# Optimization experiments

Hardware: AMD Instinct MI355X
Metric: run time of the kernel (lower is better)

The kernel has to match this reference:

```python
import jax, jax.numpy as jnp
import numpy as np

N = 129      # num_of_nodes hardcoded in EvolveGCNH(129, in_channels)
IN = 129     # in_channels; must satisfy ceil(IN/129 * N) == IN for GRU shapes
OUT = 64     # out_channels of final linear
E = 4096     # number of edges (avg degree ~32)


def setup_inputs() -> dict:
    key = jax.random.key(0)
    ks = jax.random.split(key, 12)
    s = 1.0 / np.sqrt(IN)
    x = jax.random.normal(ks[0], (N, IN), jnp.float32)
    edge_index = jax.random.randint(ks[1], (2, E), 0, N)
    edge_weight = jax.random.uniform(ks[2], (E,), jnp.float32, minval=0.1, maxval=1.0)
    # TopKPooling projection vector p
    pool_p = jax.random.normal(ks[3], (IN,), jnp.float32) * s
    # initial GCN weight (GRU hidden state), glorot-ish
    W0 = jax.random.normal(ks[4], (IN, IN), jnp.float32) * s
    # GRU parameters (torch layout: rows ordered [reset; update; new])
    w_ih = jax.random.normal(ks[5], (3 * IN, IN), jnp.float32) * s
    w_hh = jax.random.normal(ks[6], (3 * IN, IN), jnp.float32) * s
    b_ih = jax.random.normal(ks[7], (3 * IN,), jnp.float32) * s
    b_hh = jax.random.normal(ks[8], (3 * IN,), jnp.float32) * s
    conv_bias = jax.random.normal(ks[9], (IN,), jnp.float32) * s
    lin_w = jax.random.normal(ks[10], (OUT, IN), jnp.float32) * s
    lin_b = jax.random.normal(ks[11], (OUT,), jnp.float32) * s
    return {"x": x, "edge_index": edge_index, "edge_weight": edge_weight,
            "pool_p": pool_p, "W0": W0, "w_ih": w_ih, "w_hh": w_hh,
            "b_ih": b_ih, "b_hh": b_hh, "conv_bias": conv_bias,
            "lin_w": lin_w, "lin_b": lin_b}


def reference(x, edge_index, edge_weight, pool_p, W0, w_ih, w_hh, b_ih, b_hh,
              conv_bias, lin_w, lin_b):
    n = x.shape[0]
    # F.dropout in eval mode (training=False) -> identity.

    # --- TopKPooling: score = tanh(x @ p / ||p||); select top-k (k == IN == N) ---
    score = jnp.tanh((x @ pool_p) / jnp.linalg.norm(pool_p))
    perm = jnp.argsort(-score)                     # descending, k = IN = n
    x_tilde = x[perm] * score[perm][:, None]       # [k, IN]

    # --- GRU step: input batch = k pooled nodes, hidden = evolving weight W0 [IN, IN] ---
    gi = x_tilde @ w_ih.T + b_ih                   # [k, 3*IN]
    gh = W0 @ w_hh.T + b_hh                        # [IN, 3*IN]
    ir, iz, i_n = jnp.split(gi, 3, axis=1)
    hr, hz, h_n = jnp.split(gh, 3, axis=1)
    r = jax.nn.sigmoid(ir + hr)
    z = jax.nn.sigmoid(iz + hz)
    cand = jnp.tanh(i_n + r * h_n)
    W = (1.0 - z) * cand + z * W0                  # evolved GCN weight [IN, IN]

    # --- GCNConv_Fixed_W: gcn_norm with self-loops, then D^-1/2 A D^-1/2 (x @ W) ---
    row, col = edge_index[0], edge_index[1]        # source, target
    loop = jnp.arange(n)
    row_f = jnp.concatenate([row, loop])
    col_f = jnp.concatenate([col, loop])
    ew_f = jnp.concatenate([edge_weight, jnp.ones((n,), x.dtype)])
    deg = jax.ops.segment_sum(ew_f, col_f, num_segments=n)
    dis = jnp.where(deg > 0, jax.lax.rsqrt(jnp.maximum(deg, 1e-12)), 0.0)
    norm = dis[row_f] * ew_f * dis[col_f]          # [E+n]
    xw = x @ W                                     # [N, IN]
    out = jax.ops.segment_sum(norm[:, None] * xw[row_f], col_f, num_segments=n)
    out = out + conv_bias

    # --- ELU + Linear ---
    h = jax.nn.elu(out)
    return h @ lin_w.T + lin_b
```

## Files before the change

### kernel.cpp

```cpp
#include <hip/hip_runtime.h>
#include <math.h>

#define NN 129
#define INC 129
#define OUTC 64
#define NE 4096
#define WCAP 32

__device__ __forceinline__ float sigmf(float x) { return 1.0f / (1.0f + expf(-x)); }

__global__ __launch_bounds__(1024) void k_prep(
    const float* __restrict__ x, const int* __restrict__ ei,
    const float* __restrict__ ew, const float* __restrict__ p,
    float* __restrict__ score, int* __restrict__ perm, float* __restrict__ agg)
{
    int b = blockIdx.x, t = threadIdx.x;
    int wv = t >> 6, lane = t & 63;
    const int* row = ei;
    const int* col = ei + NE;

    if (b == 0) {
        __shared__ float s_sc[NN];

        float pv0 = p[lane];
        float pv1 = p[lane + 64];
        float pv2 = p[128];
        float pn = pv0 * pv0 + pv1 * pv1;
        if (lane == 0) pn += pv2 * pv2;

        float acc[9];
        #pragma unroll
        for (int k = 0; k < 9; ++k) {
            int n = wv + k * 16;
            float a = 0.f;
            if (n < NN) {
                const float* xr = x + (size_t)n * INC;
                a = xr[lane] * pv0 + xr[lane + 64] * pv1;
                if (lane == 0) a += xr[128] * pv2;
            }
            acc[k] = a;
        }
        #pragma unroll
        for (int o = 32; o; o >>= 1) {
            #pragma unroll
            for (int k = 0; k < 9; ++k) acc[k] += __shfl_xor(acc[k], o, 64);
            pn += __shfl_xor(pn, o, 64);
        }
        float rinv = 1.0f / sqrtf(pn);
        if (lane == 0) {
            #pragma unroll
            for (int k = 0; k < 9; ++k) {
                int n = wv + k * 16;
                if (n < NN) s_sc[n] = acc[k];
            }
        }
        __syncthreads();
        if (t < NN) {
            float sc = tanhf(s_sc[t] * rinv);
            s_sc[t] = sc;
            score[t] = sc;
        }
        __syncthreads();
        if (t < NN) {
            float my = s_sc[t];
            int rank = 0;
            #pragma unroll 16
            for (int j = 0; j < NN; ++j) {
                float o = s_sc[j];
                rank += (o > my || (o == my && j < t)) ? 1 : 0;
            }
            perm[rank] = t;
        }
    } else {
        int c = b - 1;
        __shared__ float s_deg[NN];
        __shared__ float s_dis[NN];
        __shared__ int   s_r[16 * WCAP];
        __shared__ float s_w[16 * WCAP];
        __shared__ int   s_cnt[16];
        __shared__ int   s_off[17];
        __shared__ int   s_dr[16 * WCAP];
        __shared__ float s_nrm[16 * WCAP];

        if (t < NN) s_deg[t] = 0.f;
        __syncthreads();
        for (int e = t; e < NE; e += 1024) atomicAdd(&s_deg[col[e]], ew[e]);
        __syncthreads();
        if (t < NN) s_dis[t] = rsqrtf(fmaxf(s_deg[t] + 1.0f, 1e-12f));
        __syncthreads();

        int basee = wv * 256;
        int cnt = 0;
        #pragma unroll
        for (int it = 0; it < 4; ++it) {
            int e = basee + it * 64 + lane;
            int rr = row[e];
            float wval = ew[e];
            bool m = (col[e] == c);
            unsigned long long mask = __ballot(m);
            if (m) {
                int pos = cnt + __popcll(mask & ((1ull << lane) - 1));
                if (pos < WCAP) { s_r[wv * WCAP + pos] = rr; s_w[wv * WCAP + pos] = wval; }
            }
            cnt += __popcll(mask);
        }
        if (lane == 0) s_cnt[wv] = min(cnt, WCAP);
        __syncthreads();
        if (t == 0) {
            int acc = 0;
            for (int w = 0; w < 16; ++w) { s_off[w] = acc; acc += s_cnt[w]; }
            s_off[16] = acc;
        }
        __syncthreads();
        float dc = s_dis[c];
        if (lane < s_cnt[wv]) {
            int r = s_r[wv * WCAP + lane];
            s_dr[s_off[wv] + lane]  = r;
            s_nrm[s_off[wv] + lane] = s_dis[r] * s_w[wv * WCAP + lane] * dc;
        }
        __syncthreads();
        int tot = s_off[16];
        if (t < NN) {
            float a = dc * dc * x[(size_t)c * INC + t];
            #pragma unroll 8
            for (int k = 0; k < tot; ++k)
                a += s_nrm[k] * x[(size_t)s_dr[k] * INC + t];
            agg[(size_t)c * INC + t] = a;
        }
    }
}

__global__ __launch_bounds__(256) void k_gru(
    const float* __restrict__ x, const float* __restrict__ score,
    const int* __restrict__ perm, const float* __restrict__ W0,
    const float* __restrict__ w_ih, const float* __restrict__ w_hh,
    const float* __restrict__ b_ih, const float* __restrict__ b_hh,
    float* __restrict__ W)
{
    int lane = threadIdx.x & 63;
    int wid = blockIdx.x * 4 + (threadIdx.x >> 6);
    if (wid >= NN * INC) return;
    int j = wid / NN;
    int i = wid - j * NN;
    int pi = perm[i];
    float sc = score[pi];
    const float* xr = x  + (size_t)pi * INC;
    const float* h0 = W0 + (size_t)i * INC;
    const float* wr = w_ih + (size_t)j * INC;
    const float* wz = wr + (size_t)INC * INC;
    const float* wn = wz + (size_t)INC * INC;
    const float* vr = w_hh + (size_t)j * INC;
    const float* vz = vr + (size_t)INC * INC;
    const float* vn = vz + (size_t)INC * INC;

    float sr = 0.f, szv = 0.f, an = 0.f, hn = 0.f;
    for (int c = lane; c < INC; c += 64) {
        float xv = xr[c] * sc;
        float hv = h0[c];
        sr  += xv * wr[c] + hv * vr[c];
        szv += xv * wz[c] + hv * vz[c];
        an  += xv * wn[c];
        hn  += hv * vn[c];
    }
    for (int o = 32; o; o >>= 1) {
        sr  += __shfl_xor(sr,  o, 64);
        szv += __shfl_xor(szv, o, 64);
        an  += __shfl_xor(an,  o, 64);
        hn  += __shfl_xor(hn,  o, 64);
    }
    if (lane == 0) {
        float r    = sigmf(sr  + b_ih[j]           + b_hh[j]);
        float z    = sigmf(szv + b_ih[INC + j]     + b_hh[INC + j]);
        float cand = tanhf(an + b_ih[2 * INC + j] + r * (hn + b_hh[2 * INC + j]));
        W[(size_t)i * INC + j] = (1.0f - z) * cand + z * h0[j];
    }
}

__global__ __launch_bounds__(1024) void k_fin(
    const float* __restrict__ agg, const float* __restrict__ W,
    const float* __restrict__ cb, const float* __restrict__ lw,
    const float* __restrict__ lb, float* __restrict__ out)
{
    __shared__ float s_a[NN];
    __shared__ float s_g[NN];
    __shared__ float s_h[NN];
    int c = blockIdx.x, t = threadIdx.x;
    int wv = t >> 6, lane = t & 63;

    if (t < NN) { s_a[t] = agg[(size_t)c * INC + t]; s_g[t] = cb[t]; }
    __syncthreads();

    float p0 = 0.f, p1 = 0.f, p2 = 0.f;
    for (int cc = wv; cc < NN; cc += 16) {
        float av = s_a[cc];
        const float* wr = W + (size_t)cc * INC;
        p0 += av * wr[lane];
        p1 += av * wr[lane + 64];
        if (lane == 0) p2 += av * wr[128];
    }
    atomicAdd(&s_g[lane], p0);
    atomicAdd(&s_g[lane + 64], p1);
    if (lane == 0) atomicAdd(&s_g[128], p2);
    __syncthreads();
    if (t < NN) { float g = s_g[t]; s_h[t] = (g > 0.f) ? g : expm1f(g); }
    __syncthreads();

    for (int f = wv; f < OUTC; f += 16) {
        const float* wrow = lw + (size_t)f * INC;
        float a = 0.f;
        for (int cc = lane; cc < INC; cc += 64) a += s_h[cc] * wrow[cc];
        for (int o = 32; o; o >>= 1) a += __shfl_xor(a, o, 64);
        if (lane == 0) out[(size_t)c * OUTC + f] = a + lb[f];
    }
}

extern "C" void kernel_launch(void* const* d_in, const int* in_sizes, int n_in,
                              void* d_out, int out_size, void* d_ws, size_t ws_size,
                              hipStream_t stream)
{
    const float* x   = (const float*)d_in[0];
    const int*   ei  = (const int*)d_in[1];
    const float* ew  = (const float*)d_in[2];
    const float* pp  = (const float*)d_in[3];
    const float* W0  = (const float*)d_in[4];
    const float* wih = (const float*)d_in[5];
    const float* whh = (const float*)d_in[6];
    const float* bih = (const float*)d_in[7];
    const float* bhh = (const float*)d_in[8];
    const float* cb  = (const float*)d_in[9];
    const float* lw  = (const float*)d_in[10];
    const float* lb  = (const float*)d_in[11];
    float* out = (float*)d_out;

    char* ws = (char*)d_ws;
    float* score = (float*)(ws + 0);
    int*   perm  = (int*)  (ws + 640);
    float* W     = (float*)(ws + 2048);
    float* agg   = (float*)(ws + 2048 + 69632);

    k_prep<<<NN + 1, 1024, 0, stream>>>(x, ei, ew, pp, score, perm, agg);

    int gru_blocks = (NN * INC + 3) / 4;
    k_gru<<<gru_blocks, 256, 0, stream>>>(x, score, perm, W0, wih, whh, bih, bhh, W);

    k_fin<<<NN, 1024, 0, stream>>>(agg, W, cb, lw, lb, out);
}
```

Measured before the change: 32.57 us.

## Move aggregation into GRU kernel and use half-wave dot products for GRU

The score/top-k step now runs as its own single-block kernel. The graph aggregation blocks are merged into the GRU launch, with 256-thread blocks instead of 1024. The GRU dot products now use 32 lanes per (i,j) output instead of a full 64-lane wave, which halves idle lanes for the 129-length reductions. Aggregation now has 4 waves each scanning 1024 edges, with the per-wave edge cap raised to 64, and the score kernel becomes a separate serial launch.

```diff
diff --git a/kernel.cpp b/kernel.cpp
--- a/kernel.cpp
+++ b/kernel.cpp
@@ -5,94 +5,106 @@
 #define INC 129
 #define OUTC 64
 #define NE 4096
-#define WCAP 32
+#define WCAP 64
+#define GRU_HW_PER_BLK 8
+#define GRU_BLKS ((NN * INC + GRU_HW_PER_BLK - 1) / GRU_HW_PER_BLK)
 
 __device__ __forceinline__ float sigmf(float x) { return 1.0f / (1.0f + expf(-x)); }
 
-__global__ __launch_bounds__(1024) void k_prep(
+__global__ __launch_bounds__(1024) void k_score(
+    const float* __restrict__ x, const float* __restrict__ p,
+    float* __restrict__ score, int* __restrict__ perm)
+{
+    int t = threadIdx.x;
+    int wv = t >> 6, lane = t & 63;
+    __shared__ float s_sc[NN];
+
+    float pv0 = p[lane];
+    float pv1 = p[lane + 64];
+    float pv2 = p[128];
+    float pn = pv0 * pv0 + pv1 * pv1;
+    if (lane == 0) pn += pv2 * pv2;
+
+    float acc[9];
+    #pragma unroll
+    for (int k = 0; k < 9; ++k) {
+        int n = wv + k * 16;
+        float a = 0.f;
+        if (n < NN) {
+            const float* xr = x + (size_t)n * INC;
+            a = xr[lane] * pv0 + xr[lane + 64] * pv1;
+            if (lane == 0) a += xr[128] * pv2;
+        }
+        acc[k] = a;
+    }
+    #pragma unroll
+    for (int o = 32; o; o >>= 1) {
+        #pragma unroll
+        for (int k = 0; k < 9; ++k) acc[k] += __shfl_xor(acc[k], o, 64);
+        pn += __shfl_xor(pn, o, 64);
+    }
+    float rinv = 1.0f / sqrtf(pn);
+    if (lane == 0) {
+        #pragma unroll
+        for (int k = 0; k < 9; ++k) {
+            int n = wv + k * 16;
+            if (n < NN) s_sc[n] = acc[k];
+        }
+    }
+    __syncthreads();
+    if (t < NN) {
+        float sc = tanhf(s_sc[t] * rinv);
+        s_sc[t] = sc;
+        score[t] = sc;
+    }
+    __syncthreads();
+    if (t < NN) {
+        float my = s_sc[t];
+        int rank = 0;
+        #pragma unroll 16
+        for (int j = 0; j < NN; ++j) {
+            float o = s_sc[j];
+            rank += (o > my || (o == my && j < t)) ? 1 : 0;
+        }
+        perm[rank] = t;
+    }
+}
+
+__global__ __launch_bounds__(256) void k_mid(
     const float* __restrict__ x, const int* __restrict__ ei,
-    const float* __restrict__ ew, const float* __restrict__ p,
-    float* __restrict__ score, int* __restrict__ perm, float* __restrict__ agg)
+    const float* __restrict__ ew, const float* __restrict__ score,
+    const int* __restrict__ perm, const float* __restrict__ W0,
+    const float* __restrict__ w_ih, const float* __restrict__ w_hh,
+    const float* __restrict__ b_ih, const float* __restrict__ b_hh,
+    float* __restrict__ W, float* __restrict__ agg)
 {
     int b = blockIdx.x, t = threadIdx.x;
     int wv = t >> 6, lane = t & 63;
     const int* row = ei;
     const int* col = ei + NE;
 
-    if (b == 0) {
-        __shared__ float s_sc[NN];
-
-        float pv0 = p[lane];
-        float pv1 = p[lane + 64];
-        float pv2 = p[128];
-        float pn = pv0 * pv0 + pv1 * pv1;
-        if (lane == 0) pn += pv2 * pv2;
-
-        float acc[9];
-        #pragma unroll
-        for (int k = 0; k < 9; ++k) {
-            int n = wv + k * 16;
-            float a = 0.f;
-            if (n < NN) {
-                const float* xr = x + (size_t)n * INC;
-                a = xr[lane] * pv0 + xr[lane + 64] * pv1;
-                if (lane == 0) a += xr[128] * pv2;
-            }
-            acc[k] = a;
-        }
-        #pragma unroll
-        for (int o = 32; o; o >>= 1) {
-            #pragma unroll
-            for (int k = 0; k < 9; ++k) acc[k] += __shfl_xor(acc[k], o, 64);
-            pn += __shfl_xor(pn, o, 64);
-        }
-        float rinv = 1.0f / sqrtf(pn);
-        if (lane == 0) {
-            #pragma unroll
-            for (int k = 0; k < 9; ++k) {
-                int n = wv + k * 16;
-                if (n < NN) s_sc[n] = acc[k];
-            }
-        }
-        __syncthreads();
-        if (t < NN) {
-            float sc = tanhf(s_sc[t] * rinv);
-            s_sc[t] = sc;
-            score[t] = sc;
-        }
-        __syncthreads();
-        if (t < NN) {
-            float my = s_sc[t];
-            int rank = 0;
-            #pragma unroll 16
-            for (int j = 0; j < NN; ++j) {
-                float o = s_sc[j];
-                rank += (o > my || (o == my && j < t)) ? 1 : 0;
-            }
-            perm[rank] = t;
-        }
-    } else {
-        int c = b - 1;
+    if (b < NN) {
+        int c = b;
         __shared__ float s_deg[NN];
         __shared__ float s_dis[NN];
-        __shared__ int   s_r[16 * WCAP];
-        __shared__ float s_w[16 * WCAP];
-        __shared__ int   s_cnt[16];
-        __shared__ int   s_off[17];
-        __shared__ int   s_dr[16 * WCAP];
-        __shared__ float s_nrm[16 * WCAP];
+        __shared__ int   s_r[4 * WCAP];
+        __shared__ float s_w[4 * WCAP];
+        __shared__ int   s_cnt[4];
+        __shared__ int   s_off[5];
+        __shared__ int   s_dr[4 * WCAP];
+        __shared__ float s_nrm[4 * WCAP];
 
         if (t < NN) s_deg[t] = 0.f;
         __syncthreads();
-        for (int e = t; e < NE; e += 1024) atomicAdd(&s_deg[col[e]], ew[e]);
+        for (int e = t; e < NE; e += 256) atomicAdd(&s_deg[col[e]], ew[e]);
         __syncthreads();
         if (t < NN) s_dis[t] = rsqrtf(fmaxf(s_deg[t] + 1.0f, 1e-12f));
         __syncthreads();
 
-        int basee = wv * 256;
+        int basee = wv * 1024;
         int cnt = 0;
         #pragma unroll
-        for (int it = 0; it < 4; ++it) {
+        for (int it = 0; it < 16; ++it) {
             int e = basee + it * 64 + lane;
             int rr = row[e];
             float wval = ew[e];
@@ -108,8 +120,8 @@
         __syncthreads();
         if (t == 0) {
             int acc = 0;
-            for (int w = 0; w < 16; ++w) { s_off[w] = acc; acc += s_cnt[w]; }
-            s_off[16] = acc;
+            for (int w = 0; w < 4; ++w) { s_off[w] = acc; acc += s_cnt[w]; }
+            s_off[4] = acc;
         }
         __syncthreads();
         float dc = s_dis[c];
@@ -119,7 +131,7 @@
             s_nrm[s_off[wv] + lane] = s_dis[r] * s_w[wv * WCAP + lane] * dc;
         }
         __syncthreads();
-        int tot = s_off[16];
+        int tot = s_off[4];
         if (t < NN) {
             float a = dc * dc * x[(size_t)c * INC + t];
             #pragma unroll 8
@@ -127,52 +139,45 @@
                 a += s_nrm[k] * x[(size_t)s_dr[k] * INC + t];
             agg[(size_t)c * INC + t] = a;
         }
-    }
-}
-
-__global__ __launch_bounds__(256) void k_gru(
-    const float* __restrict__ x, const float* __restrict__ score,
-    const int* __restrict__ perm, const float* __restrict__ W0,
-    const float* __restrict__ w_ih, const float* __restrict__ w_hh,
-    const float* __restrict__ b_ih, const float* __restrict__ b_hh,
-    float* __restrict__ W)
-{
-    int lane = threadIdx.x & 63;
-    int wid = blockIdx.x * 4 + (threadIdx.x >> 6);
-    if (wid >= NN * INC) return;
-    int j = wid / NN;
-    int i = wid - j * NN;
-    int pi = perm[i];
-    float sc = score[pi];
-    const float* xr = x  + (size_t)pi * INC;
-    const float* h0 = W0 + (size_t)i * INC;
-    const float* wr = w_ih + (size_t)j * INC;
-    const float* wz = wr + (size_t)INC * INC;
-    const float* wn = wz + (size_t)INC * INC;
-    const float* vr = w_hh + (size_t)j * INC;
-    const float* vz = vr + (size_t)INC * INC;
-    const float* vn = vz + (size_t)INC * INC;
-
-    float sr = 0.f, szv = 0.f, an = 0.f, hn = 0.f;
-    for (int c = lane; c < INC; c += 64) {
-        float xv = xr[c] * sc;
-        float hv = h0[c];
-        sr  += xv * wr[c] + hv * vr[c];
-        szv += xv * wz[c] + hv * vz[c];
-        an  += xv * wn[c];
-        hn  += hv * vn[c];
-    }
-    for (int o = 32; o; o >>= 1) {
-        sr  += __shfl_xor(sr,  o, 64);
-        szv += __shfl_xor(szv, o, 64);
-        an  += __shfl_xor(an,  o, 64);
-        hn  += __shfl_xor(hn,  o, 64);
-    }
-    if (lane == 0) {
-        float r    = sigmf(sr  + b_ih[j]           + b_hh[j]);
-        float z    = sigmf(szv + b_ih[INC + j]     + b_hh[INC + j]);
-        float cand = tanhf(an + b_ih[2 * INC + j] + r * (hn + b_hh[2 * INC + j]));
-        W[(size_t)i * INC + j] = (1.0f - z) * cand + z * h0[j];
+    } else {
+        int hw = (b - NN) * GRU_HW_PER_BLK + (wv << 1) + (lane >> 5);
+        if (hw >= NN * INC) return;
+        int l32 = lane & 31;
+        int j = hw / NN;
+        int i = hw - j * NN;
+        int pi = perm[i];
+        float sc = score[pi];
+        const float* xr = x  + (size_t)pi * INC;
+        const float* h0 = W0 + (size_t)i * INC;
+        const float* wr = w_ih + (size_t)j * INC;
+        const float* wz = wr + (size_t)INC * INC;
+        const float* wn = wz + (size_t)INC * INC;
+        const float* vr = w_hh + (size_t)j * INC;
+        const float* vz = vr + (size_t)INC * INC;
+        const float* vn = vz + (size_t)INC * INC;
+
+        float sr = 0.f, szv = 0.f, an = 0.f, hn = 0.f;
+        for (int c = l32; c < INC; c += 32) {
+            float xv = xr[c] * sc;
+            float hv = h0[c];
+            sr  += xv * wr[c] + hv * vr[c];
+            szv += xv * wz[c] + hv * vz[c];
+            an  += xv * wn[c];
+            hn  += hv * vn[c];
+        }
+        #pragma unroll
+        for (int o = 16; o; o >>= 1) {
+            sr  += __shfl_xor(sr,  o, 32);
+            szv += __shfl_xor(szv, o, 32);
+            an  += __shfl_xor(an,  o, 32);
+            hn  += __shfl_xor(hn,  o, 32);
+        }
+        if (l32 == 0) {
+            float r    = sigmf(sr  + b_ih[j]           + b_hh[j]);
+            float z    = sigmf(szv + b_ih[INC + j]     + b_hh[INC + j]);
+            float cand = tanhf(an + b_ih[2 * INC + j] + r * (hn + b_hh[2 * INC + j]));
+            W[(size_t)i * INC + j] = (1.0f - z) * cand + z * h0[j];
+        }
     }
 }
 
@@ -238,10 +243,10 @@
     float* W     = (float*)(ws + 2048);
     float* agg   = (float*)(ws + 2048 + 69632);
 
-    k_prep<<<NN + 1, 1024, 0, stream>>>(x, ei, ew, pp, score, perm, agg);
-
-    int gru_blocks = (NN * INC + 3) / 4;
-    k_gru<<<gru_blocks, 256, 0, stream>>>(x, score, perm, W0, wih, whh, bih, bhh, W);
+    k_score<<<1, 1024, 0, stream>>>(x, pp, score, perm);
+
+    k_mid<<<NN + GRU_BLKS, 256, 0, stream>>>(
+        x, ei, ew, score, perm, W0, wih, whh, bih, bhh, W, agg);
 
     k_fin<<<NN, 1024, 0, stream>>>(agg, W, cb, lw, lb, out);
 }
```

After: 35.52 us. 1.09x slower.
